# Performance work log

Hardware: AMD Instinct MI355X
Metric: run time of the kernel (lower is better)

## Reference

```python
import jax, jax.numpy as jnp
import numpy as np
from jax.scipy.linalg import expm

N, T, IN, C, M = 64, 2048, 8, 2, 10  # batch, time, input_size, channels, hidden_size


def setup_inputs() -> dict:
    key = jax.random.key(0)
    k1, k2 = jax.random.split(key)
    x = jax.random.normal(k1, (N, T, IN), dtype=jnp.float32)
    # Lie-algebra generator parameters; small init keeps expm well-conditioned
    A = jax.random.normal(k2, (C, IN, M, M), dtype=jnp.float32) * (1.0 / (M * IN))
    return {"x": x, "A": A}


def dyadic_prod(X):
    # X: (N, T, C, m, m) -> cumulative (ordered) matrix product over time: (N, C, m, m)
    n, t, c, m, _ = X.shape
    levels = int(np.ceil(np.log2(t)))
    I = jnp.broadcast_to(jnp.eye(m, dtype=X.dtype), (n, 1, c, m, m))
    for _ in range(levels):
        if X.shape[1] % 2 == 1:
            X = jnp.concatenate([X, I], axis=1)  # pad with identity
        Xp = X.reshape(n, -1, 2, c, m, m)
        X = jnp.einsum('ntcij,ntcjk->ntcik', Xp[:, :, 0], Xp[:, :, 1])
    return X[:, 0]


def reference(x, A):
    # Skew-symmetrize generators -> so(m) Lie algebra elements, per channel/input dim
    skew = A - jnp.swapaxes(A, -1, -2)          # (C, IN, m, m)
    dX = x[:, 1:] - x[:, :-1]                   # (N, T-1, IN) path increments
    G = jnp.einsum('nti,cijk->ntcjk', dX, skew) # (N, T-1, C, m, m)
    Mexp = expm(G)                              # batched matrix exponential -> SO(m)
    return dyadic_prod(Mexp)                    # (N, C, m, m)
```

## Files before the change

### kernel.cpp

```cpp
#include <hip/hip_runtime.h>

#define NB     64
#define TT     2048
#define INQ    8
#define CC     2
#define MM     10
#define ROWP   12
#define MATS   124
#define PSTR   20
#define SLEN   8
#define SEGS   64
#define NCHUNK 4
#define NCHAIN (NB*CC)

typedef float v2f __attribute__((ext_vector_type(2)));

__device__ __forceinline__ constexpr int triIdx(int k, int j) {
    return k * 10 + j - ((k + 1) * (k + 2)) / 2;
}

template <int SRC>
__device__ __forceinline__ float dpp_qbcast(float v) {
    const int i = __float_as_int(v);
    const int r = __builtin_amdgcn_update_dpp(i, i, SRC * 0x55, 0xF, 0xF, true);
    return __int_as_float(r);
}

__device__ __forceinline__ void pair_combine(float* buf_s, int ls, int rs, int pq) {
    float lrow[5][MM];
    #pragma unroll
    for (int r = 0; r < 5; ++r) {
        const float4* lr = reinterpret_cast<const float4*>(
            &buf_s[ls * MATS + (pq * 5 + r) * ROWP]);
        const float4 a = lr[0], b = lr[1], c4 = lr[2];
        lrow[r][0] = a.x;  lrow[r][1] = a.y;  lrow[r][2] = a.z;  lrow[r][3] = a.w;
        lrow[r][4] = b.x;  lrow[r][5] = b.y;  lrow[r][6] = b.z;  lrow[r][7] = b.w;
        lrow[r][8] = c4.x; lrow[r][9] = c4.y;
    }
    float d[5][MM];
    #pragma unroll
    for (int r = 0; r < 5; ++r)
        #pragma unroll
        for (int j = 0; j < MM; ++j)
            d[r][j] = 0.0f;
    #pragma unroll
    for (int k = 0; k < MM; ++k) {
        const float4* rr = reinterpret_cast<const float4*>(&buf_s[rs * MATS + k * ROWP]);
        const float4 a = rr[0], b = rr[1], c4 = rr[2];
        float rrow[MM];
        rrow[0] = a.x;  rrow[1] = a.y;  rrow[2] = a.z;  rrow[3] = a.w;
        rrow[4] = b.x;  rrow[5] = b.y;  rrow[6] = b.z;  rrow[7] = b.w;
        rrow[8] = c4.x; rrow[9] = c4.y;
        #pragma unroll
        for (int r = 0; r < 5; ++r) {
            const float lv = lrow[r][k];
            #pragma unroll
            for (int j = 0; j < MM; ++j)
                d[r][j] += lv * rrow[j];
        }
    }
    float* dst = &buf_s[ls * MATS + pq * 5 * ROWP];
    #pragma unroll
    for (int r = 0; r < 5; ++r) {
        float4* drow = reinterpret_cast<float4*>(dst + r * ROWP);
        drow[0] = make_float4(d[r][0], d[r][1], d[r][2], d[r][3]);
        drow[1] = make_float4(d[r][4], d[r][5], d[r][6], d[r][7]);
        drow[2] = make_float4(d[r][8], d[r][9], 0.0f, 0.0f);
    }
}

__global__ __launch_bounds__(256)
void dev_serial(const float* __restrict__ x,
                const float* __restrict__ A,
                float* __restrict__ ws)
{
    __shared__ __align__(16) float skp_s[24 * PSTR];
    __shared__ __align__(16) float buf_s[SEGS * MATS];

    const int tid   = threadIdx.x;
    const int chain = blockIdx.x >> 2;
    const int qt    = blockIdx.x & 3;
    const int n     = chain >> 1;
    const int c     = chain & 1;

    for (int e = tid; e < 24 * 16; e += 256) {
        const int p   = e >> 4;
        const int rem = e & 15;
        const int ip  = rem >> 1;
        const int h   = rem & 1;
        const int t   = 2 * p + h;
        float v = 0.0f;
        if (t < 45) {
            int k = 0, r2 = t;
            while (r2 >= 9 - k) { r2 -= (9 - k); ++k; }
            const int j = k + 1 + r2;
            const float* Ab = A + (size_t)(c * INQ + ip) * (MM * MM);
            v = Ab[k * MM + j] - Ab[j * MM + k];
        }
        skp_s[p * PSTR + 2 * ip + h] = v;
    }
    for (int p = tid; p < 24; p += 256) {
        skp_s[p * PSTR + 16] = 0.0f; skp_s[p * PSTR + 17] = 0.0f;
        skp_s[p * PSTR + 18] = 0.0f; skp_s[p * PSTR + 19] = 0.0f;
    }
    __syncthreads();

    const int seg = tid >> 2;
    const int q   = tid & 3;
    const int p0  = (q < 2) ? 3 * q : (q == 2 ? 6 : 8);
    const int sr  = (q < 2) ? (3 * q + 2) : 9;
    const bool hasS = (q < 2);

    v2f   R01[MM];
    float R2[MM];
    #pragma unroll
    for (int j = 0; j < MM; ++j) {
        R01[j] = (v2f){ (j == p0) ? 1.0f : 0.0f, (j == p0 + 1) ? 1.0f : 0.0f };
        R2[j]  = (j == sr) ? 1.0f : 0.0f;
    }

    const float* xb = x + (size_t)n * TT * INQ;
    const int t0 = qt * (SEGS * SLEN) + seg * SLEN;

    float4 cur0, cur1, nxt0, nxt1;
    {
        const float4* p = reinterpret_cast<const float4*>(xb + (size_t)t0 * INQ);
        cur0 = p[0]; cur1 = p[1];
        int t1 = t0 + 1; if (t1 > TT - 1) t1 = TT - 1;
        const float4* pn = reinterpret_cast<const float4*>(xb + (size_t)t1 * INQ);
        nxt0 = pn[0]; nxt1 = pn[1];
    }

    #pragma unroll 1
    for (int s = 0; s < SLEN; ++s) {
        float dx[INQ];
        dx[0] = nxt0.x - cur0.x; dx[1] = nxt0.y - cur0.y;
        dx[2] = nxt0.z - cur0.z; dx[3] = nxt0.w - cur0.w;
        dx[4] = nxt1.x - cur1.x; dx[5] = nxt1.y - cur1.y;
        dx[6] = nxt1.z - cur1.z; dx[7] = nxt1.w - cur1.w;
        cur0 = nxt0; cur1 = nxt1;
        {
            int t2 = t0 + s + 2; if (t2 > TT - 1) t2 = TT - 1;
            const float4* pn = reinterpret_cast<const float4*>(xb + (size_t)t2 * INQ);
            nxt0 = pn[0]; nxt1 = pn[1];
        }

        v2f tvp[6];
        #pragma unroll
        for (int pp = 0; pp < 6; ++pp) {
            const v2f* sp = reinterpret_cast<const v2f*>(&skp_s[(6 * q + pp) * PSTR]);
            v2f acc = dx[0] * sp[0];
            #pragma unroll
            for (int ip = 1; ip < INQ; ++ip)
                acc += dx[ip] * sp[ip];
            tvp[pp] = acc;
        }
        float tv[12];
        #pragma unroll
        for (int pp = 0; pp < 6; ++pp) { tv[2 * pp] = tvp[pp].x; tv[2 * pp + 1] = tvp[pp].y; }

        float Tri[45];
        #define TRIFILL(U) Tri[U] = dpp_qbcast<(U) / 12>(tv[(U) % 12]);
        TRIFILL(0)  TRIFILL(1)  TRIFILL(2)  TRIFILL(3)  TRIFILL(4)
        TRIFILL(5)  TRIFILL(6)  TRIFILL(7)  TRIFILL(8)  TRIFILL(9)
        TRIFILL(10) TRIFILL(11) TRIFILL(12) TRIFILL(13) TRIFILL(14)
        TRIFILL(15) TRIFILL(16) TRIFILL(17) TRIFILL(18) TRIFILL(19)
        TRIFILL(20) TRIFILL(21) TRIFILL(22) TRIFILL(23) TRIFILL(24)
        TRIFILL(25) TRIFILL(26) TRIFILL(27) TRIFILL(28) TRIFILL(29)
        TRIFILL(30) TRIFILL(31) TRIFILL(32) TRIFILL(33) TRIFILL(34)
        TRIFILL(35) TRIFILL(36) TRIFILL(37) TRIFILL(38) TRIFILL(39)
        TRIFILL(40) TRIFILL(41) TRIFILL(42) TRIFILL(43) TRIFILL(44)
        #undef TRIFILL

        v2f   Acc01[MM];
        float Acc2[MM];

        #define TAYLOR_TERM(S01, S2, CJ)                                      \
        {                                                                     \
            v2f   t01[MM];                                                    \
            float t2[MM];                                                     \
            t01[0] = -S01[1] * Tri[triIdx(0, 1)];                             \
            t2[0]  = -S2[1]  * Tri[triIdx(0, 1)];                             \
            _Pragma("unroll")                                                 \
            for (int j = 1; j < MM; ++j) {                                    \
                t01[j] = S01[0] * Tri[triIdx(0, j)];                          \
                t2[j]  = S2[0]  * Tri[triIdx(0, j)];                          \
            }                                                                 \
            _Pragma("unroll")                                                 \
            for (int k = 1; k < MM; ++k) {                                    \
                const v2f   a01 = S01[k];                                     \
                const float a2  = S2[k];                                      \
                _Pragma("unroll")                                             \
                for (int j = 0; j < MM; ++j) {                                \
                    if (k == j) continue;                                     \
                    if (j == 0 && k == 1) continue;                           \
                    if (j > k) {                                              \
                        const float t = Tri[triIdx(k, j)];                    \
                        t01[j] += a01 * t;                                    \
                        t2[j]  += a2 * t;                                     \
                    } else {                                                  \
                        const float t = Tri[triIdx(j, k)];                    \
                        t01[j] -= a01 * t;                                    \
                        t2[j]  -= a2 * t;                                     \
                    }                                                         \
                }                                                             \
            }                                                                 \
            _Pragma("unroll")                                                 \
            for (int j = 0; j < MM; ++j) {                                    \
                Acc01[j] = t01[j];                                            \
                Acc2[j]  = t2[j];                                             \
                R01[j]  += CJ * t01[j];                                       \
                R2[j]   += CJ * t2[j];                                        \
            }                                                                 \
        }

        TAYLOR_TERM(R01,   R2,   1.0f)
        TAYLOR_TERM(Acc01, Acc2, 0.5f)
        TAYLOR_TERM(Acc01, Acc2, 0.16666667f)
        TAYLOR_TERM(Acc01, Acc2, 0.041666668f)
        TAYLOR_TERM(Acc01, Acc2, 0.0083333338f)
        TAYLOR_TERM(Acc01, Acc2, 0.0013888889f)
        #undef TAYLOR_TERM
    }

    {
        float* dst = &buf_s[seg * MATS];
        float4* d0 = reinterpret_cast<float4*>(dst + p0 * ROWP);
        d0[0] = make_float4(R01[0].x, R01[1].x, R01[2].x, R01[3].x);
        d0[1] = make_float4(R01[4].x, R01[5].x, R01[6].x, R01[7].x);
        d0[2] = make_float4(R01[8].x, R01[9].x, 0.0f, 0.0f);
        float4* d1 = reinterpret_cast<float4*>(dst + (p0 + 1) * ROWP);
        d1[0] = make_float4(R01[0].y, R01[1].y, R01[2].y, R01[3].y);
        d1[1] = make_float4(R01[4].y, R01[5].y, R01[6].y, R01[7].y);
        d1[2] = make_float4(R01[8].y, R01[9].y, 0.0f, 0.0f);
        if (hasS) {
            float4* d2 = reinterpret_cast<float4*>(dst + sr * ROWP);
            d2[0] = make_float4(R2[0], R2[1], R2[2], R2[3]);
            d2[1] = make_float4(R2[4], R2[5], R2[6], R2[7]);
            d2[2] = make_float4(R2[8], R2[9], 0.0f, 0.0f);
        }
    }
    __syncthreads();

    #pragma unroll 1
    for (int span = 2; span <= SEGS; span <<= 1) {
        const int np = SEGS / span;
        if (tid < 2 * np) {
            const int pr = tid >> 1;
            const int pq = tid & 1;
            pair_combine(buf_s, pr * span, pr * span + (span >> 1), pq);
        }
        __syncthreads();
    }

    if (tid < 30) {
        const float4 v = reinterpret_cast<const float4*>(buf_s)[tid];
        reinterpret_cast<float4*>(ws)[((size_t)chain * NCHUNK + qt) * 30 + tid] = v;
    }
}

__global__ __launch_bounds__(256)
void dev_tree4(const float* __restrict__ ws, float* __restrict__ out)
{
    __shared__ __align__(16) float buf_s[4 * MATS];
    const int tid   = threadIdx.x;
    const int chain = blockIdx.x;

    if (tid < 120) {
        const int m  = tid / 30;
        const int o4 = tid - m * 30;
        const float4 v = reinterpret_cast<const float4*>(ws)[((size_t)chain * 4 + m) * 30 + o4];
        reinterpret_cast<float4*>(&buf_s[m * MATS])[o4] = v;
    }
    __syncthreads();

    if (tid < 4)
        pair_combine(buf_s, (tid >> 1) * 2, (tid >> 1) * 2 + 1, tid & 1);
    __syncthreads();
    if (tid < 2)
        pair_combine(buf_s, 0, 2, tid);
    __syncthreads();

    if (tid < 100) {
        const int i = tid / 10;
        const int j = tid - i * 10;
        out[(size_t)chain * 100 + tid] = buf_s[i * ROWP + j];
    }
}

extern "C" void kernel_launch(void* const* d_in, const int* in_sizes, int n_in,
                              void* d_out, int out_size, void* d_ws, size_t ws_size,
                              hipStream_t stream) {
    (void)in_sizes; (void)n_in; (void)out_size; (void)ws_size;
    const float* x = (const float*)d_in[0];
    const float* A = (const float*)d_in[1];
    float* out = (float*)d_out;
    float* ws  = (float*)d_ws;

    dev_serial<<<dim3(NCHAIN * NCHUNK), dim3(256), 0, stream>>>(x, A, ws);
    dev_tree4<<<dim3(NCHAIN), dim3(256), 0, stream>>>(ws, out);
}
```

Before: 115.0 us.

## Split each matrix across two lanes and halve serial segment length

```diff
diff --git a/kernel.cpp b/kernel.cpp
--- a/kernel.cpp
+++ b/kernel.cpp
@@ -8,8 +8,8 @@
 #define ROWP   12
 #define MATS   124
 #define PSTR   20
-#define SLEN   8
-#define SEGS   64
+#define SLEN   4
+#define SEGS   128
 #define NCHUNK 4
 #define NCHAIN (NB*CC)
 
@@ -19,11 +19,52 @@
     return k * 10 + j - ((k + 1) * (k + 2)) / 2;
 }
 
-template <int SRC>
-__device__ __forceinline__ float dpp_qbcast(float v) {
+__device__ __forceinline__ float dpp_xor1(float v) {
     const int i = __float_as_int(v);
-    const int r = __builtin_amdgcn_update_dpp(i, i, SRC * 0x55, 0xF, 0xF, true);
+    const int r = __builtin_amdgcn_update_dpp(i, i, 0xB1, 0xF, 0xF, true);
     return __int_as_float(r);
+}
+
+__device__ __forceinline__ void trow_pk(const float* __restrict__ Tri,
+                                        v2f* A, v2f* R, const v2f* S, float cj) {
+    v2f t[MM];
+    t[0] = -S[1] * Tri[triIdx(0, 1)];
+    #pragma unroll
+    for (int j = 1; j < MM; ++j) t[j] = S[0] * Tri[triIdx(0, j)];
+    #pragma unroll
+    for (int k = 1; k < MM; ++k) {
+        const v2f a = S[k];
+        #pragma unroll
+        for (int j = 0; j < MM; ++j) {
+            if (k == j) continue;
+            if (j == 0 && k == 1) continue;
+            if (j > k) t[j] += a * Tri[triIdx(k, j)];
+            else       t[j] -= a * Tri[triIdx(j, k)];
+        }
+    }
+    #pragma unroll
+    for (int j = 0; j < MM; ++j) { A[j] = t[j]; R[j] += cj * t[j]; }
+}
+
+__device__ __forceinline__ void trow_s(const float* __restrict__ Tri,
+                                       float* A, float* R, const float* S, float cj) {
+    float t[MM];
+    t[0] = -S[1] * Tri[triIdx(0, 1)];
+    #pragma unroll
+    for (int j = 1; j < MM; ++j) t[j] = S[0] * Tri[triIdx(0, j)];
+    #pragma unroll
+    for (int k = 1; k < MM; ++k) {
+        const float a = S[k];
+        #pragma unroll
+        for (int j = 0; j < MM; ++j) {
+            if (k == j) continue;
+            if (j == 0 && k == 1) continue;
+            if (j > k) t[j] += a * Tri[triIdx(k, j)];
+            else       t[j] -= a * Tri[triIdx(j, k)];
+        }
+    }
+    #pragma unroll
+    for (int j = 0; j < MM; ++j) { A[j] = t[j]; R[j] += cj * t[j]; }
 }
 
 __device__ __forceinline__ void pair_combine(float* buf_s, int ls, int rs, int pq) {
@@ -84,11 +125,11 @@
     const int c     = chain & 1;
 
     for (int e = tid; e < 24 * 16; e += 256) {
-        const int p   = e >> 4;
+        const int r   = e >> 4;
         const int rem = e & 15;
         const int ip  = rem >> 1;
         const int h   = rem & 1;
-        const int t   = 2 * p + h;
+        const int t   = 24 * (r / 12) + 2 * (r % 12) + h;
         float v = 0.0f;
         if (t < 45) {
             int k = 0, r2 = t;
@@ -97,26 +138,25 @@
             const float* Ab = A + (size_t)(c * INQ + ip) * (MM * MM);
             v = Ab[k * MM + j] - Ab[j * MM + k];
         }
-        skp_s[p * PSTR + 2 * ip + h] = v;
-    }
-    for (int p = tid; p < 24; p += 256) {
-        skp_s[p * PSTR + 16] = 0.0f; skp_s[p * PSTR + 17] = 0.0f;
-        skp_s[p * PSTR + 18] = 0.0f; skp_s[p * PSTR + 19] = 0.0f;
+        skp_s[r * PSTR + 2 * ip + h] = v;
+    }
+    for (int r = tid; r < 24; r += 256) {
+        skp_s[r * PSTR + 16] = 0.0f; skp_s[r * PSTR + 17] = 0.0f;
+        skp_s[r * PSTR + 18] = 0.0f; skp_s[r * PSTR + 19] = 0.0f;
     }
     __syncthreads();
 
-    const int seg = tid >> 2;
-    const int q   = tid & 3;
-    const int p0  = (q < 2) ? 3 * q : (q == 2 ? 6 : 8);
-    const int sr  = (q < 2) ? (3 * q + 2) : 9;
-    const bool hasS = (q < 2);
-
-    v2f   R01[MM];
-    float R2[MM];
+    const int seg = tid >> 1;
+    const int p   = tid & 1;
+    const int r5  = 5 * p;
+
+    v2f   Rp0[MM], Rp1[MM];
+    float Rs[MM];
     #pragma unroll
     for (int j = 0; j < MM; ++j) {
-        R01[j] = (v2f){ (j == p0) ? 1.0f : 0.0f, (j == p0 + 1) ? 1.0f : 0.0f };
-        R2[j]  = (j == sr) ? 1.0f : 0.0f;
+        Rp0[j] = (v2f){ (j == r5)     ? 1.0f : 0.0f, (j == r5 + 1) ? 1.0f : 0.0f };
+        Rp1[j] = (v2f){ (j == r5 + 2) ? 1.0f : 0.0f, (j == r5 + 3) ? 1.0f : 0.0f };
+        Rs[j]  = (j == r5 + 4) ? 1.0f : 0.0f;
     }
 
     const float* xb = x + (size_t)n * TT * INQ;
@@ -124,8 +164,8 @@
 
     float4 cur0, cur1, nxt0, nxt1;
     {
-        const float4* p = reinterpret_cast<const float4*>(xb + (size_t)t0 * INQ);
-        cur0 = p[0]; cur1 = p[1];
+        const float4* pp = reinterpret_cast<const float4*>(xb + (size_t)t0 * INQ);
+        cur0 = pp[0]; cur1 = pp[1];
         int t1 = t0 + 1; if (t1 > TT - 1) t1 = TT - 1;
         const float4* pn = reinterpret_cast<const float4*>(xb + (size_t)t1 * INQ);
         nxt0 = pn[0]; nxt1 = pn[1];
@@ -145,22 +185,23 @@
             nxt0 = pn[0]; nxt1 = pn[1];
         }
 
-        v2f tvp[6];
-        #pragma unroll
-        for (int pp = 0; pp < 6; ++pp) {
-            const v2f* sp = reinterpret_cast<const v2f*>(&skp_s[(6 * q + pp) * PSTR]);
+        float tv[24];
+        #pragma unroll
+        for (int pp = 0; pp < 12; ++pp) {
+            const v2f* sp = reinterpret_cast<const v2f*>(&skp_s[(p * 12 + pp) * PSTR]);
             v2f acc = dx[0] * sp[0];
             #pragma unroll
             for (int ip = 1; ip < INQ; ++ip)
                 acc += dx[ip] * sp[ip];
-            tvp[pp] = acc;
-        }
-        float tv[12];
-        #pragma unroll
-        for (int pp = 0; pp < 6; ++pp) { tv[2 * pp] = tvp[pp].x; tv[2 * pp + 1] = tvp[pp].y; }
+            tv[2 * pp] = acc.x; tv[2 * pp + 1] = acc.y;
+        }
 
         float Tri[45];
-        #define TRIFILL(U) Tri[U] = dpp_qbcast<(U) / 12>(tv[(U) % 12]);
+        #define TRIFILL(U) {                                                   \
+            const float own = tv[(U) % 24];                                    \
+            const float rec = dpp_xor1(own);                                   \
+            Tri[U] = ((U) / 24 == 0) ? (p ? rec : own) : (p ? own : rec);      \
+        }
         TRIFILL(0)  TRIFILL(1)  TRIFILL(2)  TRIFILL(3)  TRIFILL(4)
         TRIFILL(5)  TRIFILL(6)  TRIFILL(7)  TRIFILL(8)  TRIFILL(9)
         TRIFILL(10) TRIFILL(11) TRIFILL(12) TRIFILL(13) TRIFILL(14)
@@ -172,78 +213,55 @@
         TRIFILL(40) TRIFILL(41) TRIFILL(42) TRIFILL(43) TRIFILL(44)
         #undef TRIFILL
 
-        v2f   Acc01[MM];
-        float Acc2[MM];
-
-        #define TAYLOR_TERM(S01, S2, CJ)                                      \
-        {                                                                     \
-            v2f   t01[MM];                                                    \
-            float t2[MM];                                                     \
-            t01[0] = -S01[1] * Tri[triIdx(0, 1)];                             \
-            t2[0]  = -S2[1]  * Tri[triIdx(0, 1)];                             \
-            _Pragma("unroll")                                                 \
-            for (int j = 1; j < MM; ++j) {                                    \
-                t01[j] = S01[0] * Tri[triIdx(0, j)];                          \
-                t2[j]  = S2[0]  * Tri[triIdx(0, j)];                          \
-            }                                                                 \
-            _Pragma("unroll")                                                 \
-            for (int k = 1; k < MM; ++k) {                                    \
-                const v2f   a01 = S01[k];                                     \
-                const float a2  = S2[k];                                      \
-                _Pragma("unroll")                                             \
-                for (int j = 0; j < MM; ++j) {                                \
-                    if (k == j) continue;                                     \
-                    if (j == 0 && k == 1) continue;                           \
-                    if (j > k) {                                              \
-                        const float t = Tri[triIdx(k, j)];                    \
-                        t01[j] += a01 * t;                                    \
-                        t2[j]  += a2 * t;                                     \
-                    } else {                                                  \
-                        const float t = Tri[triIdx(j, k)];                    \
-                        t01[j] -= a01 * t;                                    \
-                        t2[j]  -= a2 * t;                                     \
-                    }                                                         \
-                }                                                             \
-            }                                                                 \
-            _Pragma("unroll")                                                 \
-            for (int j = 0; j < MM; ++j) {                                    \
-                Acc01[j] = t01[j];                                            \
-                Acc2[j]  = t2[j];                                             \
-                R01[j]  += CJ * t01[j];                                       \
-                R2[j]   += CJ * t2[j];                                        \
-            }                                                                 \
-        }
-
-        TAYLOR_TERM(R01,   R2,   1.0f)
-        TAYLOR_TERM(Acc01, Acc2, 0.5f)
-        TAYLOR_TERM(Acc01, Acc2, 0.16666667f)
-        TAYLOR_TERM(Acc01, Acc2, 0.041666668f)
-        TAYLOR_TERM(Acc01, Acc2, 0.0083333338f)
-        TAYLOR_TERM(Acc01, Acc2, 0.0013888889f)
-        #undef TAYLOR_TERM
+        v2f   Ap0[MM], Ap1[MM];
+        float As[MM];
+        trow_pk(Tri, Ap0, Rp0, Rp0, 1.0f);
+        trow_pk(Tri, Ap1, Rp1, Rp1, 1.0f);
+        trow_s (Tri, As,  Rs,  Rs,  1.0f);
+        trow_pk(Tri, Ap0, Rp0, Ap0, 0.5f);
+        trow_pk(Tri, Ap1, Rp1, Ap1, 0.5f);
+        trow_s (Tri, As,  Rs,  As,  0.5f);
+        trow_pk(Tri, Ap0, Rp0, Ap0, 0.16666667f);
+        trow_pk(Tri, Ap1, Rp1, Ap1, 0.16666667f);
+        trow_s (Tri, As,  Rs,  As,  0.16666667f);
+        trow_pk(Tri, Ap0, Rp0, Ap0, 0.041666668f);
+        trow_pk(Tri, Ap1, Rp1, Ap1, 0.041666668f);
+        trow_s (Tri, As,  Rs,  As,  0.041666668f);
+        trow_pk(Tri, Ap0, Rp0, Ap0, 0.0083333338f);
+        trow_pk(Tri, Ap1, Rp1, Ap1, 0.0083333338f);
+        trow_s (Tri, As,  Rs,  As,  0.0083333338f);
+        trow_pk(Tri, Ap0, Rp0, Ap0, 0.0013888889f);
+        trow_pk(Tri, Ap1, Rp1, Ap1, 0.0013888889f);
+        trow_s (Tri, As,  Rs,  As,  0.0013888889f);
     }
 
     {
         float* dst = &buf_s[seg * MATS];
-        float4* d0 = reinterpret_cast<float4*>(dst + p0 * ROWP);
-        d0[0] = make_float4(R01[0].x, R01[1].x, R01[2].x, R01[3].x);
-        d0[1] = make_float4(R01[4].x, R01[5].x, R01[6].x, R01[7].x);
-        d0[2] = make_float4(R01[8].x, R01[9].x, 0.0f, 0.0f);
-        float4* d1 = reinterpret_cast<float4*>(dst + (p0 + 1) * ROWP);
-        d1[0] = make_float4(R01[0].y, R01[1].y, R01[2].y, R01[3].y);
-        d1[1] = make_float4(R01[4].y, R01[5].y, R01[6].y, R01[7].y);
-        d1[2] = make_float4(R01[8].y, R01[9].y, 0.0f, 0.0f);
-        if (hasS) {
-            float4* d2 = reinterpret_cast<float4*>(dst + sr * ROWP);
-            d2[0] = make_float4(R2[0], R2[1], R2[2], R2[3]);
-            d2[1] = make_float4(R2[4], R2[5], R2[6], R2[7]);
-            d2[2] = make_float4(R2[8], R2[9], 0.0f, 0.0f);
-        }
+        float4* d0 = reinterpret_cast<float4*>(dst + (r5 + 0) * ROWP);
+        d0[0] = make_float4(Rp0[0].x, Rp0[1].x, Rp0[2].x, Rp0[3].x);
+        d0[1] = make_float4(Rp0[4].x, Rp0[5].x, Rp0[6].x, Rp0[7].x);
+        d0[2] = make_float4(Rp0[8].x, Rp0[9].x, 0.0f, 0.0f);
+        float4* d1 = reinterpret_cast<float4*>(dst + (r5 + 1) * ROWP);
+        d1[0] = make_float4(Rp0[0].y, Rp0[1].y, Rp0[2].y, Rp0[3].y);
+        d1[1] = make_float4(Rp0[4].y, Rp0[5].y, Rp0[6].y, Rp0[7].y);
+        d1[2] = make_float4(Rp0[8].y, Rp0[9].y, 0.0f, 0.0f);
+        float4* d2 = reinterpret_cast<float4*>(dst + (r5 + 2) * ROWP);
+        d2[0] = make_float4(Rp1[0].x, Rp1[1].x, Rp1[2].x, Rp1[3].x);
+        d2[1] = make_float4(Rp1[4].x, Rp1[5].x, Rp1[6].x, Rp1[7].x);
+        d2[2] = make_float4(Rp1[8].x, Rp1[9].x, 0.0f, 0.0f);
+        float4* d3 = reinterpret_cast<float4*>(dst + (r5 + 3) * ROWP);
+        d3[0] = make_float4(Rp1[0].y, Rp1[1].y, Rp1[2].y, Rp1[3].y);
+        d3[1] = make_float4(Rp1[4].y, Rp1[5].y, Rp1[6].y, Rp1[7].y);
+        d3[2] = make_float4(Rp1[8].y, Rp1[9].y, 0.0f, 0.0f);
+        float4* d4 = reinterpret_cast<float4*>(dst + (r5 + 4) * ROWP);
+        d4[0] = make_float4(Rs[0], Rs[1], Rs[2], Rs[3]);
+        d4[1] = make_float4(Rs[4], Rs[5], Rs[6], Rs[7]);
+        d4[2] = make_float4(Rs[8], Rs[9], 0.0f, 0.0f);
     }
     __syncthreads();
 
     #pragma unroll 1
-    for (int span = 2; span <= SEGS; span <<= 1) {
+    for (int span = 2; span <= 64; span <<= 1) {
         const int np = SEGS / span;
         if (tid < 2 * np) {
             const int pr = tid >> 1;
@@ -253,33 +271,39 @@
         __syncthreads();
     }
 
-    if (tid < 30) {
-        const float4 v = reinterpret_cast<const float4*>(buf_s)[tid];
-        reinterpret_cast<float4*>(ws)[((size_t)chain * NCHUNK + qt) * 30 + tid] = v;
+    if (tid < 60) {
+        const int m  = tid / 30;
+        const int o4 = tid - m * 30;
+        const float4 v = reinterpret_cast<const float4*>(&buf_s[(m * 64) * MATS])[o4];
+        reinterpret_cast<float4*>(ws)[(((size_t)chain * 4 + qt) * 2 + m) * 30 + o4] = v;
     }
 }
 
 __global__ __launch_bounds__(256)
-void dev_tree4(const float* __restrict__ ws, float* __restrict__ out)
+void dev_tree8(const float* __restrict__ ws, float* __restrict__ out)
 {
-    __shared__ __align__(16) float buf_s[4 * MATS];
+    __shared__ __align__(16) float buf_s[8 * MATS];
     const int tid   = threadIdx.x;
     const int chain = blockIdx.x;
 
-    if (tid < 120) {
+    if (tid < 240) {
         const int m  = tid / 30;
         const int o4 = tid - m * 30;
-        const float4 v = reinterpret_cast<const float4*>(ws)[((size_t)chain * 4 + m) * 30 + o4];
+        const float4 v = reinterpret_cast<const float4*>(ws)[((size_t)chain * 8 + m) * 30 + o4];
         reinterpret_cast<float4*>(&buf_s[m * MATS])[o4] = v;
     }
     __syncthreads();
 
-    if (tid < 4)
-        pair_combine(buf_s, (tid >> 1) * 2, (tid >> 1) * 2 + 1, tid & 1);
-    __syncthreads();
-    if (tid < 2)
-        pair_combine(buf_s, 0, 2, tid);
-    __syncthreads();
+    #pragma unroll 1
+    for (int span = 2; span <= 8; span <<= 1) {
+        const int np = 8 / span;
+        if (tid < 2 * np) {
+            const int pr = tid >> 1;
+            const int pq = tid & 1;
+            pair_combine(buf_s, pr * span, pr * span + (span >> 1), pq);
+        }
+        __syncthreads();
+    }
 
     if (tid < 100) {
         const int i = tid / 10;
@@ -298,5 +322,5 @@
     float* ws  = (float*)d_ws;
 
     dev_serial<<<dim3(NCHAIN * NCHUNK), dim3(256), 0, stream>>>(x, A, ws);
-    dev_tree4<<<dim3(NCHAIN), dim3(256), 0, stream>>>(ws, out);
-}
+    dev_tree8<<<dim3(NCHAIN), dim3(256), 0, stream>>>(ws, out);
+}
```

Result: slower. 120.4 us (+4.7%).
